# Optimization experiments

Hardware: AMD Instinct MI355X
Metric: run time of the kernel (lower is better)

Reference implementation:

```python
import jax, jax.numpy as jnp
import numpy as np

DIM = 1024
NUM_HEADS = 16
HEAD_DIM = DIM // NUM_HEADS
SCALE = HEAD_DIM ** -0.5


def setup_inputs() -> dict:
    key = jax.random.key(0)
    k1, k2, k3 = jax.random.split(key, 3)
    B, S = 4, 2048
    x = jax.random.normal(k1, (B, S, DIM), dtype=jnp.float32)
    w_qkv = jax.random.normal(k2, (DIM, 3 * DIM), dtype=jnp.float32) * (DIM ** -0.5)
    b_qkv = jnp.zeros((3 * DIM,), dtype=jnp.float32)
    w_proj = jax.random.normal(k3, (DIM, DIM), dtype=jnp.float32) * (DIM ** -0.5)
    b_proj = jnp.zeros((DIM,), dtype=jnp.float32)
    return {"x": x, "w_qkv": w_qkv, "b_qkv": b_qkv, "w_proj": w_proj, "b_proj": b_proj}


def reference(x, w_qkv, b_qkv, w_proj, b_proj):
    B, S, D = x.shape
    # QKV projection: [B,S,3D] -> [3,B,H,S,hd]
    qkv = x @ w_qkv + b_qkv
    qkv = qkv.reshape(B, S, 3, NUM_HEADS, HEAD_DIM).transpose(2, 0, 3, 1, 4)
    q, k, v = qkv[0], qkv[1], qkv[2]
    # scores: [B,H,S,S]
    scores = jnp.einsum("bhqd,bhkd->bhqk", q, k) * SCALE
    attn = jax.nn.softmax(scores, axis=-1)
    # weighted average: [B,H,S,hd] -> [B,S,D]
    out = jnp.einsum("bhqk,bhkd->bhqd", attn, v)
    out = out.transpose(0, 2, 1, 3).reshape(B, S, D)
    return out @ w_proj + b_proj
```

## Files before the change

kernel.cpp:

```cpp
#include <hip/hip_runtime.h>
#include <stdint.h>

typedef unsigned short u16;
typedef __attribute__((ext_vector_type(8))) short bf16x8;
typedef __attribute__((ext_vector_type(4))) float f32x4;
typedef __attribute__((ext_vector_type(2))) uint32_t u32x2;

#define NHEADS 16
#define HD 64
#define BATCH 4
#define SEQ 2048
#define DMODEL 1024
#define QSCALE_LOG2E 0.18033688011112042f

__device__ __forceinline__ u16 f2bf(float f) {
  union { float f; uint32_t u; } v; v.f = f;
  uint32_t r = v.u + 0x7FFFu + ((v.u >> 16) & 1u);
  return (u16)(r >> 16);
}
__device__ __forceinline__ float exp2_fast(float x) {
  float r;
  asm("v_exp_f32 %0, %1" : "=v"(r) : "v"(x));
  return r;
}
__device__ __forceinline__ uint32_t cvt_pk_bf16(float lo, float hi) {
  uint32_t r;
  asm("v_cvt_pk_bf16_f32 %0, %1, %2" : "=v"(r) : "v"(lo), "v"(hi));
  return r;
}
__device__ __forceinline__ uint32_t swz(uint32_t r, uint32_t c) {
  return r * 128u + ((c ^ (r & 7u)) << 4);
}
__device__ __forceinline__ uint32_t swz_elem(uint32_t r, uint32_t col) {
  return r * 128u + (((col >> 3) ^ (r & 7u)) << 4) + ((col & 7u) << 1);
}

__global__ void transpose_k(const float* __restrict__ in, u16* __restrict__ out,
                            int R, int C) {
  __shared__ float t[32][33];
  const int bc = blockIdx.x * 32, br = blockIdx.y * 32;
  const int x = threadIdx.x, y = threadIdx.y;
#pragma unroll
  for (int i = 0; i < 32; i += 8) t[y + i][x] = in[(size_t)(br + y + i) * C + bc + x];
  __syncthreads();
#pragma unroll
  for (int i = 0; i < 32; i += 8) out[(size_t)(bc + y + i) * R + br + x] = f2bf(t[x][y + i]);
}

__global__ __launch_bounds__(256) void f32_to_bf16(const float* __restrict__ in,
                                                   u16* __restrict__ out) {
  const size_t i = ((size_t)blockIdx.x * 256 + threadIdx.x) * 8;
  const f32x4 v0 = *(const f32x4*)(in + i);
  const f32x4 v1 = *(const f32x4*)(in + i + 4);
  bf16x8 b;
#pragma unroll
  for (int j = 0; j < 4; ++j) { b[j] = (short)f2bf(v0[j]); b[4 + j] = (short)f2bf(v1[j]); }
  *(bf16x8*)(out + i) = b;
}

template <int MODE>
__global__ __launch_bounds__(256) void gemm_bt(const u16* __restrict__ A,
                                               const u16* __restrict__ Bt,
                                               const float* __restrict__ bias,
                                               void* __restrict__ Cv,
                                               int M, int N, int K) {
  __shared__ u16 Alds[128 * 64];
  __shared__ u16 Blds[128 * 64];
  const int tid = threadIdx.x;
  const int w = tid >> 6, lane = tid & 63;
  const int wr = w >> 1, wc = w & 1;
  const int lr = lane & 15, lg = lane >> 4;

  const int nwg = gridDim.x;
  int bid = blockIdx.x;
  bid = (bid & 7) * (nwg >> 3) + (bid >> 3);
  const int nx = N >> 7;
  const int col0 = (bid % nx) * 128, row0 = (bid / nx) * 128;

  const int r8 = lane >> 3;
  const int csrc = ((lane & 7) ^ r8) * 8;

  f32x4 acc[4][4];
#pragma unroll
  for (int m = 0; m < 4; ++m)
#pragma unroll
    for (int n = 0; n < 4; ++n) acc[m][n] = (f32x4){0.f, 0.f, 0.f, 0.f};

  for (int k0 = 0; k0 < K; k0 += 64) {
#pragma unroll
    for (int p = 0; p < 4; ++p) {
      const int r = p * 32 + w * 8 + r8;
      const int g0 = (p * 256 + w * 64) * 8;
      __builtin_amdgcn_global_load_lds(
          (const __attribute__((address_space(1))) void*)(A + (size_t)(row0 + r) * K + k0 + csrc),
          (__attribute__((address_space(3))) void*)(&Alds[g0]), 16, 0, 0);
      __builtin_amdgcn_global_load_lds(
          (const __attribute__((address_space(1))) void*)(Bt + (size_t)(col0 + r) * K + k0 + csrc),
          (__attribute__((address_space(3))) void*)(&Blds[g0]), 16, 0, 0);
    }
    asm volatile("s_waitcnt vmcnt(0)" ::: "memory");
    __syncthreads();
#pragma unroll
    for (int kk = 0; kk < 2; ++kk) {
      bf16x8 af[4], bfr[4];
#pragma unroll
      for (int m = 0; m < 4; ++m)
        af[m] = *(const bf16x8*)((char*)Alds + swz(wr * 64 + m * 16 + lr, kk * 4 + lg));
#pragma unroll
      for (int n = 0; n < 4; ++n)
        bfr[n] = *(const bf16x8*)((char*)Blds + swz(wc * 64 + n * 16 + lr, kk * 4 + lg));
#pragma unroll
      for (int m = 0; m < 4; ++m)
#pragma unroll
        for (int n = 0; n < 4; ++n)
          acc[m][n] = __builtin_amdgcn_mfma_f32_16x16x32_bf16(af[m], bfr[n], acc[m][n], 0, 0, 0);
    }
    __syncthreads();
  }

#pragma unroll
  for (int m = 0; m < 4; ++m) {
#pragma unroll
    for (int n = 0; n < 4; ++n) {
      const int col = col0 + wc * 64 + n * 16 + lr;
      const float bv = bias[col];
#pragma unroll
      for (int r = 0; r < 4; ++r) {
        const int row = row0 + wr * 64 + m * 16 + lg * 4 + r;
        float v = acc[m][n][r] + bv;
        if (MODE == 0) {
          ((float*)Cv)[(size_t)row * N + col] = v;
        } else {
          const int which = col >> 10;
          if (which == 0) v *= QSCALE_LOG2E;
          const int hcol = col & 1023;
          const int h = hcol >> 6, d = hcol & 63;
          const int b = row >> 11, s = row & 2047;
          size_t off;
          if (which == 2) {
            off = (size_t)2 * (BATCH * NHEADS * SEQ * HD) +
                  (((size_t)b * NHEADS + h) * HD + d) * SEQ + s;
          } else {
            off = (size_t)which * (BATCH * NHEADS * SEQ * HD) +
                  ((((size_t)b * NHEADS + h) * SEQ + s) * HD) + d;
          }
          ((u16*)Cv)[off] = f2bf(v);
        }
      }
    }
  }
}

__global__ __launch_bounds__(256) void attn_fwd(const u16* __restrict__ Qg,
                                                const u16* __restrict__ Kg,
                                                const u16* __restrict__ Vtg,
                                                u16* __restrict__ Og) {
  __shared__ u16 KV[2][2][64 * 64];
  __shared__ u16 Plds[4][2][16 * 64];
  const int tid = threadIdx.x;
  const int w = tid >> 6, lane = tid & 63;
  const int lr = lane & 15, lg = lane >> 4;

  int bid = blockIdx.x;
  bid = (bid & 7) * ((BATCH * NHEADS * SEQ / 128) >> 3) + (bid >> 3);
  const int bh = bid >> 4;
  const int q0 = (bid & 15) * 128;
  const size_t base = (size_t)bh * (SEQ * HD);

  bf16x8 qf[2][2];
#pragma unroll
  for (int sub = 0; sub < 2; ++sub)
#pragma unroll
    for (int kk = 0; kk < 2; ++kk)
      qf[sub][kk] = *(const bf16x8*)(Qg + base +
          (size_t)(q0 + w * 32 + sub * 16 + lr) * HD + kk * 32 + lg * 8);

  const short one_bf = (short)0x3F80;
  const bf16x8 ones = {one_bf, one_bf, one_bf, one_bf, one_bf, one_bf, one_bf, one_bf};

  f32x4 acc[2][4], accl[2];
#pragma unroll
  for (int sub = 0; sub < 2; ++sub) {
#pragma unroll
    for (int nf = 0; nf < 4; ++nf) acc[sub][nf] = (f32x4){0.f, 0.f, 0.f, 0.f};
    accl[sub] = (f32x4){0.f, 0.f, 0.f, 0.f};
  }

  const int r8 = lane >> 3;
  const int csrc = ((lane & 7) ^ r8) * 8;

#define STAGE(BUF, T)                                                              \
  {                                                                                \
    const int s0_ = (T) * 64;                                                      \
    _Pragma("unroll")                                                              \
    for (int ch = 0; ch < 2; ++ch) {                                               \
      const int q8 = w * 2 + ch;                                                   \
      const int r = q8 * 8 + r8;                                                   \
      __builtin_amdgcn_global_load_lds(                                            \
          (const __attribute__((address_space(1))) void*)(Kg + base +              \
              (size_t)(s0_ + r) * HD + csrc),                                      \
          (__attribute__((address_space(3))) void*)(&KV[BUF][0][q8 * 512]),        \
          16, 0, 0);                                                               \
      __builtin_amdgcn_global_load_lds(                                            \
          (const __attribute__((address_space(1))) void*)(Vtg + base +             \
              (size_t)r * SEQ + s0_ + csrc),                                       \
          (__attribute__((address_space(3))) void*)(&KV[BUF][1][q8 * 512]),        \
          16, 0, 0);                                                               \
    }                                                                              \
  }

  STAGE(0, 0);

  for (int t = 0; t < SEQ / 64; ++t) {
    const int buf = t & 1;
    asm volatile("s_waitcnt vmcnt(0)" ::: "memory");
    __syncthreads();
    if (t + 1 < SEQ / 64) STAGE(buf ^ 1, t + 1);

    const u16* Kl = &KV[buf][0][0];
    const u16* Vl = &KV[buf][1][0];

    f32x4 sf[2][4];
#pragma unroll
    for (int sub = 0; sub < 2; ++sub)
#pragma unroll
      for (int f = 0; f < 4; ++f) sf[sub][f] = (f32x4){0.f, 0.f, 0.f, 0.f};
    __builtin_amdgcn_s_setprio(1);
#pragma unroll
    for (int kk = 0; kk < 2; ++kk) {
#pragma unroll
      for (int f = 0; f < 4; ++f) {
        const bf16x8 kf = *(const bf16x8*)((char*)Kl + swz(f * 16 + lr, kk * 4 + lg));
        sf[0][f] = __builtin_amdgcn_mfma_f32_16x16x32_bf16(kf, qf[0][kk], sf[0][f], 0, 0, 0);
        sf[1][f] = __builtin_amdgcn_mfma_f32_16x16x32_bf16(kf, qf[1][kk], sf[1][f], 0, 0, 0);
      }
    }
    __builtin_amdgcn_s_setprio(0);

#pragma unroll
    for (int sub = 0; sub < 2; ++sub) {
#pragma unroll
      for (int f = 0; f < 4; ++f) {
#pragma unroll
        for (int r = 0; r < 4; ++r) sf[sub][f][r] = exp2_fast(sf[sub][f][r]);
        const u32x2 wv = {cvt_pk_bf16(sf[sub][f][0], sf[sub][f][1]),
                          cvt_pk_bf16(sf[sub][f][2], sf[sub][f][3])};
        *(u32x2*)((char*)&Plds[w][sub][0] + swz_elem(lr, f * 16 + lg * 4)) = wv;
      }
    }
    asm volatile("s_waitcnt lgkmcnt(0)" ::: "memory");
    __builtin_amdgcn_sched_barrier(0);

    __builtin_amdgcn_s_setprio(1);
#pragma unroll
    for (int kk = 0; kk < 2; ++kk) {
      const bf16x8 pf0 = *(const bf16x8*)((char*)&Plds[w][0][0] + swz(lr, kk * 4 + lg));
      const bf16x8 pf1 = *(const bf16x8*)((char*)&Plds[w][1][0] + swz(lr, kk * 4 + lg));
#pragma unroll
      for (int nf = 0; nf < 4; ++nf) {
        const bf16x8 vf = *(const bf16x8*)((char*)Vl + swz(nf * 16 + lr, kk * 4 + lg));
        acc[0][nf] = __builtin_amdgcn_mfma_f32_16x16x32_bf16(pf0, vf, acc[0][nf], 0, 0, 0);
        acc[1][nf] = __builtin_amdgcn_mfma_f32_16x16x32_bf16(pf1, vf, acc[1][nf], 0, 0, 0);
      }
      accl[0] = __builtin_amdgcn_mfma_f32_16x16x32_bf16(pf0, ones, accl[0], 0, 0, 0);
      accl[1] = __builtin_amdgcn_mfma_f32_16x16x32_bf16(pf1, ones, accl[1], 0, 0, 0);
    }
    __builtin_amdgcn_s_setprio(0);
  }
#undef STAGE

  const int b = bh >> 4, h = bh & 15;
#pragma unroll
  for (int sub = 0; sub < 2; ++sub) {
    float linv[4];
#pragma unroll
    for (int r = 0; r < 4; ++r) linv[r] = 1.0f / accl[sub][r];
#pragma unroll
    for (int nf = 0; nf < 4; ++nf)
#pragma unroll
      for (int r = 0; r < 4; ++r) {
        const int row = q0 + w * 32 + sub * 16 + lg * 4 + r;
        const int col = nf * 16 + lr;
        Og[((size_t)(b * SEQ + row)) * DMODEL + h * HD + col] =
            f2bf(acc[sub][nf][r] * linv[r]);
      }
  }
}

extern "C" void kernel_launch(void* const* d_in, const int* in_sizes, int n_in,
                              void* d_out, int out_size, void* d_ws, size_t ws_size,
                              hipStream_t stream) {
  const float* x      = (const float*)d_in[0];
  const float* w_qkv  = (const float*)d_in[1];
  const float* b_qkv  = (const float*)d_in[2];
  const float* w_proj = (const float*)d_in[3];
  const float* b_proj = (const float*)d_in[4];
  float* out = (float*)d_out;
  char* ws = (char*)d_ws;

  u16* wt_qkv  = (u16*)(ws);
  u16* wt_proj = (u16*)(ws + 6291456);
  u16* q       = (u16*)(ws + 8388608);
  u16* o       = (u16*)(ws + 8388608 + 3 * 16777216);
  u16* kk      = q + 8388608;
  u16* vt      = q + 2 * 8388608;
  u16* xb      = o;

  transpose_k<<<dim3(3072 / 32, 1024 / 32), dim3(32, 8), 0, stream>>>(w_qkv, wt_qkv, 1024, 3072);
  transpose_k<<<dim3(1024 / 32, 1024 / 32), dim3(32, 8), 0, stream>>>(w_proj, wt_proj, 1024, 1024);
  f32_to_bf16<<<4096, 256, 0, stream>>>(x, xb);
  gemm_bt<1><<<(3072 / 128) * (8192 / 128), 256, 0, stream>>>(xb, wt_qkv, b_qkv, q, 8192, 3072, 1024);
  attn_fwd<<<BATCH * NHEADS * SEQ / 128, 256, 0, stream>>>(q, kk, vt, o);
  gemm_bt<0><<<(1024 / 128) * (8192 / 128), 256, 0, stream>>>(o, wt_proj, b_proj, out, 8192, 1024, 1024);
}
```

Before: 226.2 us.

## Process P·V per sub-tile with a halved P buffer and pointer-incremented staging

The P·V stage now runs separately for each of the two 16-row sub-tiles. Each sub-tile does its exp, writes P to LDS, waits, then runs its MFMAs. This lets the per-wave P buffer in LDS shrink by half and keeps fewer P fragments live in registers, which may allow more resident blocks and lets exp work of one sub-tile overlap MFMA of the other. The K/V staging loads now use pointers that are precomputed and advanced by a fixed stride each tile, instead of recomputing addresses every iteration. The cost is that V fragments are read from LDS twice per tile, once per sub-tile, and there is an extra lgkmcnt wait per sub-tile.

```diff
diff --git a/kernel.cpp b/kernel.cpp
--- a/kernel.cpp
+++ b/kernel.cpp
@@ -156,7 +156,7 @@
                                                 const u16* __restrict__ Vtg,
                                                 u16* __restrict__ Og) {
   __shared__ u16 KV[2][2][64 * 64];
-  __shared__ u16 Plds[4][2][16 * 64];
+  __shared__ u16 Plds[4][16 * 64];
   const int tid = threadIdx.x;
   const int w = tid >> 6, lane = tid & 63;
   const int lr = lane & 15, lg = lane >> 4;
@@ -189,33 +189,36 @@
   const int r8 = lane >> 3;
   const int csrc = ((lane & 7) ^ r8) * 8;
 
-#define STAGE(BUF, T)                                                              \
+  const int rr = w * 16 + r8;
+  const u16* kp = Kg + base + (size_t)rr * HD + csrc;
+  const u16* vp = Vtg + base + (size_t)rr * SEQ + csrc;
+  const int d0 = (w * 2) * 512, d1 = (w * 2 + 1) * 512;
+
+#define STAGE(BUF)                                                                 \
   {                                                                                \
-    const int s0_ = (T) * 64;                                                      \
-    _Pragma("unroll")                                                              \
-    for (int ch = 0; ch < 2; ++ch) {                                               \
-      const int q8 = w * 2 + ch;                                                   \
-      const int r = q8 * 8 + r8;                                                   \
-      __builtin_amdgcn_global_load_lds(                                            \
-          (const __attribute__((address_space(1))) void*)(Kg + base +              \
-              (size_t)(s0_ + r) * HD + csrc),                                      \
-          (__attribute__((address_space(3))) void*)(&KV[BUF][0][q8 * 512]),        \
-          16, 0, 0);                                                               \
-      __builtin_amdgcn_global_load_lds(                                            \
-          (const __attribute__((address_space(1))) void*)(Vtg + base +             \
-              (size_t)r * SEQ + s0_ + csrc),                                       \
-          (__attribute__((address_space(3))) void*)(&KV[BUF][1][q8 * 512]),        \
-          16, 0, 0);                                                               \
-    }                                                                              \
-  }
-
-  STAGE(0, 0);
+    __builtin_amdgcn_global_load_lds(                                              \
+        (const __attribute__((address_space(1))) void*)(kp),                       \
+        (__attribute__((address_space(3))) void*)(&KV[BUF][0][d0]), 16, 0, 0);     \
+    __builtin_amdgcn_global_load_lds(                                              \
+        (const __attribute__((address_space(1))) void*)(kp + 8 * HD),              \
+        (__attribute__((address_space(3))) void*)(&KV[BUF][0][d1]), 16, 0, 0);     \
+    __builtin_amdgcn_global_load_lds(                                              \
+        (const __attribute__((address_space(1))) void*)(vp),                       \
+        (__attribute__((address_space(3))) void*)(&KV[BUF][1][d0]), 16, 0, 0);     \
+    __builtin_amdgcn_global_load_lds(                                              \
+        (const __attribute__((address_space(1))) void*)(vp + 8 * SEQ),             \
+        (__attribute__((address_space(3))) void*)(&KV[BUF][1][d1]), 16, 0, 0);     \
+    kp += 64 * HD;                                                                 \
+    vp += 64;                                                                      \
+  }
+
+  STAGE(0);
 
   for (int t = 0; t < SEQ / 64; ++t) {
     const int buf = t & 1;
     asm volatile("s_waitcnt vmcnt(0)" ::: "memory");
     __syncthreads();
-    if (t + 1 < SEQ / 64) STAGE(buf ^ 1, t + 1);
+    if (t + 1 < SEQ / 64) STAGE(buf ^ 1);
 
     const u16* Kl = &KV[buf][0][0];
     const u16* Vl = &KV[buf][1][0];
@@ -245,27 +248,24 @@
         for (int r = 0; r < 4; ++r) sf[sub][f][r] = exp2_fast(sf[sub][f][r]);
         const u32x2 wv = {cvt_pk_bf16(sf[sub][f][0], sf[sub][f][1]),
                           cvt_pk_bf16(sf[sub][f][2], sf[sub][f][3])};
-        *(u32x2*)((char*)&Plds[w][sub][0] + swz_elem(lr, f * 16 + lg * 4)) = wv;
-      }
-    }
-    asm volatile("s_waitcnt lgkmcnt(0)" ::: "memory");
-    __builtin_amdgcn_sched_barrier(0);
-
-    __builtin_amdgcn_s_setprio(1);
-#pragma unroll
-    for (int kk = 0; kk < 2; ++kk) {
-      const bf16x8 pf0 = *(const bf16x8*)((char*)&Plds[w][0][0] + swz(lr, kk * 4 + lg));
-      const bf16x8 pf1 = *(const bf16x8*)((char*)&Plds[w][1][0] + swz(lr, kk * 4 + lg));
-#pragma unroll
-      for (int nf = 0; nf < 4; ++nf) {
-        const bf16x8 vf = *(const bf16x8*)((char*)Vl + swz(nf * 16 + lr, kk * 4 + lg));
-        acc[0][nf] = __builtin_amdgcn_mfma_f32_16x16x32_bf16(pf0, vf, acc[0][nf], 0, 0, 0);
-        acc[1][nf] = __builtin_amdgcn_mfma_f32_16x16x32_bf16(pf1, vf, acc[1][nf], 0, 0, 0);
-      }
-      accl[0] = __builtin_amdgcn_mfma_f32_16x16x32_bf16(pf0, ones, accl[0], 0, 0, 0);
-      accl[1] = __builtin_amdgcn_mfma_f32_16x16x32_bf16(pf1, ones, accl[1], 0, 0, 0);
-    }
-    __builtin_amdgcn_s_setprio(0);
+        *(u32x2*)((char*)&Plds[w][0] + swz_elem(lr, f * 16 + lg * 4)) = wv;
+      }
+      asm volatile("s_waitcnt lgkmcnt(0)" ::: "memory");
+      __builtin_amdgcn_sched_barrier(0);
+
+      __builtin_amdgcn_s_setprio(1);
+#pragma unroll
+      for (int kk = 0; kk < 2; ++kk) {
+        const bf16x8 pf = *(const bf16x8*)((char*)&Plds[w][0] + swz(lr, kk * 4 + lg));
+#pragma unroll
+        for (int nf = 0; nf < 4; ++nf) {
+          const bf16x8 vf = *(const bf16x8*)((char*)Vl + swz(nf * 16 + lr, kk * 4 + lg));
+          acc[sub][nf] = __builtin_amdgcn_mfma_f32_16x16x32_bf16(pf, vf, acc[sub][nf], 0, 0, 0);
+        }
+        accl[sub] = __builtin_amdgcn_mfma_f32_16x16x32_bf16(pf, ones, accl[sub], 0, 0, 0);
+      }
+      __builtin_amdgcn_s_setprio(0);
+    }
   }
 #undef STAGE
 
```

Result: slower. 231.4 us (+2.3%).
